# Optimization experiments

Hardware: AMD Instinct MI355X
Metric: run time of the kernel (lower is better)

## Reference

```python
import jax, jax.numpy as jnp
import numpy as np

NEG_INF = -jnp.inf


def setup_inputs() -> dict:
    key = jax.random.key(0)
    ks = jax.random.split(key, 8)
    B, C, H, W = 8, 512, 96, 96
    IC = max(1, C // 8)  # inter_channels = 64
    s = 1.0 / np.sqrt(C)
    x = jax.random.normal(ks[0], (B, C, H, W), dtype=jnp.float32)
    Wq = jax.random.normal(ks[1], (IC, C), dtype=jnp.float32) * s
    bq = jax.random.normal(ks[2], (IC,), dtype=jnp.float32) * s
    Wk = jax.random.normal(ks[3], (IC, C), dtype=jnp.float32) * s
    bk = jax.random.normal(ks[4], (IC,), dtype=jnp.float32) * s
    Wv = jax.random.normal(ks[5], (C, C), dtype=jnp.float32) * s
    bv = jax.random.normal(ks[6], (C,), dtype=jnp.float32) * s
    gamma = jnp.full((1,), 0.5, dtype=jnp.float32)  # nn.Parameter (zeros in torch; nonzero here for a non-trivial baseline)
    return {"x": x, "Wq": Wq, "bq": bq, "Wk": Wk, "bk": bk, "Wv": Wv, "bv": bv, "gamma": gamma}


def reference(x, Wq, bq, Wk, bk, Wv, bv, gamma):
    B, C, H, W = x.shape
    # 1x1 convs as channel contractions
    q = jnp.einsum('oc,bchw->bohw', Wq, x) + bq[None, :, None, None]
    k = jnp.einsum('oc,bchw->bohw', Wk, x) + bk[None, :, None, None]
    v = jnp.einsum('oc,bchw->bohw', Wv, x) + bv[None, :, None, None]
    # column (height-axis) attention logits: [B, H, W, H'] with -inf on h==h'
    e_h = jnp.einsum('bchw,bcgw->bhwg', q, k)
    eye = jnp.eye(H, dtype=bool)[:, None, :]  # [H,1,H'] broadcast over W
    e_h = jnp.where(eye[None], NEG_INF, e_h)
    # row (width-axis) attention logits: [B, H, W, W']
    e_w = jnp.einsum('bchw,bchv->bhwv', q, k)
    # joint softmax over concatenated H'+W' axis
    attn = jax.nn.softmax(jnp.concatenate([e_h, e_w], axis=-1), axis=-1)
    a_h = attn[..., :H]   # [B,H,W,H']
    a_w = attn[..., H:]   # [B,H,W,W']
    out_h = jnp.einsum('bcgw,bhwg->bchw', v, a_h)
    out_w = jnp.einsum('bchv,bhwv->bchw', v, a_w)
    return gamma[0] * (out_h + out_w) + x
```

## Files before the change

kernel.cpp:

```cpp
#include <hip/hip_runtime.h>
#include <hip/hip_bf16.h>

typedef __hip_bfloat16 bf16;
typedef unsigned short us8 __attribute__((ext_vector_type(8)));
typedef __attribute__((ext_vector_type(8))) short short8v;
typedef __attribute__((ext_vector_type(4))) float float4v;

__device__ __forceinline__ float us2f(unsigned short u){
  return __uint_as_float(((unsigned int)u) << 16);
}
__device__ __forceinline__ float b2f(bf16 v){ return __bfloat162float(v); }
__device__ __forceinline__ bf16 f2b(float v){ return __float2bfloat16(v); }
__device__ __forceinline__ unsigned short f2bu(float v){
  bf16 t = f2b(v); return *reinterpret_cast<unsigned short*>(&t);
}

#define HW 9216
#define CH 512
#define NQ 640

__global__ void k_detect(const unsigned int* __restrict__ xw, int* __restrict__ flag){
  int t = threadIdx.x;
  int cnt = 0;
  for(int i=t;i<4096;i+=256){
    unsigned e = (xw[i]>>8)&0x7F;
    if(e==0x3E||e==0x3F) cnt++;
  }
  #pragma unroll
  for(int o=32;o>0;o>>=1) cnt += __shfl_xor(cnt,o);
  __shared__ int s[4];
  if((t&63)==0) s[t>>6]=cnt;
  __syncthreads();
  if(t==0){ int tot=s[0]+s[1]+s[2]+s[3]; *flag = (tot > 1228) ? 1 : 0; }
}

__global__ void k_pack(const void* __restrict__ Wq, const void* __restrict__ Wk,
                       const void* __restrict__ Wv, const void* __restrict__ bq,
                       const void* __restrict__ bk, const void* __restrict__ bv,
                       const int* __restrict__ flag,
                       bf16* __restrict__ Wall, float* __restrict__ ball){
  bool isbf = (*flag)!=0;
  int j = blockIdx.x, t = threadIdx.x;
  const void* src = (j < 64) ? Wq : (j < 128) ? Wk : Wv;
  int row = (j < 64) ? j : (j < 128) ? (j-64) : (j-128);
  for(int c=t;c<512;c+=256){
    float v = isbf ? b2f(((const bf16*)src)[(size_t)row*512+c])
                   : ((const float*)src)[(size_t)row*512+c];
    Wall[(size_t)j*512+c] = f2b(v);
  }
  if(t==0){
    const void* bsrc = (j<64)? bq : (j<128)? bk : bv;
    ball[j] = isbf ? b2f(((const bf16*)bsrc)[row]) : ((const float*)bsrc)[row];
  }
}

__global__ __launch_bounds__(256) void k_xcvt(const void* __restrict__ x,
    const int* __restrict__ flag, bf16* __restrict__ xT){
  __shared__ float T[64][65];
  bool isbf = (*flag)!=0;
  int b = blockIdx.z, c0 = blockIdx.y*64, hw0 = blockIdx.x*64;
  int tid = threadIdx.x;
  if(isbf){
    const bf16* xb = (const bf16*)x + ((size_t)b*CH + c0)*HW + hw0;
    #pragma unroll
    for(int i=0;i<2;i++){
      int e = i*256 + tid;
      int cc = e>>3, h8 = (e&7)*8;
      us8 v = *(const us8*)(xb + (size_t)cc*HW + h8);
      #pragma unroll
      for(int j=0;j<8;j++) T[cc][h8+j] = us2f(v[j]);
    }
  } else {
    const float* xb = (const float*)x + ((size_t)b*CH + c0)*HW + hw0;
    #pragma unroll
    for(int i=0;i<4;i++){
      int e = i*256 + tid;
      int cc = e>>4, h4 = (e&15)*4;
      float4 v = *(const float4*)(xb + (size_t)cc*HW + h4);
      T[cc][h4]=v.x; T[cc][h4+1]=v.y; T[cc][h4+2]=v.z; T[cc][h4+3]=v.w;
    }
  }
  __syncthreads();
  bf16* tb = xT + ((size_t)b*HW + hw0)*512 + c0;
  #pragma unroll
  for(int i=0;i<2;i++){
    int e = i*256 + tid;
    int r = e>>3, c8 = (e&7)*8;
    us8 o;
    #pragma unroll
    for(int j=0;j<8;j++) o[j] = f2bu(T[c8+j][r]);
    *(us8*)(tb + (size_t)r*512 + c8) = o;
  }
}

__global__ __launch_bounds__(256) void k_qkv(const bf16* __restrict__ xT,
    const bf16* __restrict__ Wall, const float* __restrict__ ball,
    bf16* __restrict__ Ot){
  __shared__ ushort As[128][72];
  __shared__ ushort Bs[128][72];
  int b = blockIdx.y;
  int bx = blockIdx.x;
  int swz = (bx & 7)*45 + (bx >> 3);
  int m0 = (swz/5)*128;
  int n0 = (swz%5)*128;
  int tid = threadIdx.x, wid = tid>>6, lane = tid&63;
  int m0w = (wid>>1)*64, n0w = (wid&1)*64;
  const bf16* Ab = xT + ((size_t)b*HW + m0)*512;
  const bf16* Bb = Wall + (size_t)n0*512;
  float4v acc[4][4];
  #pragma unroll
  for(int mt=0;mt<4;mt++)
    #pragma unroll
    for(int nt=0;nt<4;nt++) acc[mt][nt] = (float4v){0.f,0.f,0.f,0.f};
  for(int k0=0;k0<512;k0+=64){
    #pragma unroll
    for(int i=0;i<4;i++){
      int s = tid + i*256;
      int row = s>>3, ko = (s&7)*8;
      us8 v = *(const us8*)(Ab + (size_t)row*512 + k0 + ko);
      *(us8*)&As[row][ko] = v;
      us8 w = *(const us8*)(Bb + (size_t)row*512 + k0 + ko);
      *(us8*)&Bs[row][ko] = w;
    }
    __syncthreads();
    #pragma unroll
    for(int kk=0;kk<64;kk+=32){
      short8v a[4], bb[4];
      #pragma unroll
      for(int mt=0;mt<4;mt++) a[mt] = *(short8v*)&As[m0w+mt*16+(lane&15)][kk+8*(lane>>4)];
      #pragma unroll
      for(int nt=0;nt<4;nt++) bb[nt] = *(short8v*)&Bs[n0w+nt*16+(lane&15)][kk+8*(lane>>4)];
      #pragma unroll
      for(int mt=0;mt<4;mt++)
        #pragma unroll
        for(int nt=0;nt<4;nt++)
          acc[mt][nt] = __builtin_amdgcn_mfma_f32_16x16x32_bf16(a[mt], bb[nt], acc[mt][nt], 0,0,0);
    }
    __syncthreads();
  }
  #pragma unroll
  for(int mt=0;mt<4;mt++){
    #pragma unroll
    for(int nt=0;nt<4;nt++){
      int nn = n0 + n0w + nt*16 + (lane&15);
      float bias = ball[nn];
      int mbase = m0 + m0w + mt*16 + (lane>>4)*4;
      #pragma unroll
      for(int r=0;r<4;r++)
        Ot[((size_t)b*HW + mbase + r)*640 + nn] = f2b(acc[mt][nt][r] + bias);
    }
  }
}

__global__ __launch_bounds__(384) void k_eh(const bf16* __restrict__ Ot,
                                            float* __restrict__ esc){
  __shared__ ushort Qs[96][72];
  __shared__ ushort Ks[96][72];
  int b = blockIdx.y, w = blockIdx.x;
  int tid = threadIdx.x, wid = tid>>6, lane = tid&63;
  const bf16* qb = Ot + ((size_t)b*HW + w)*640;
  #pragma unroll
  for(int i=0;i<2;i++){
    int e = tid + i*384;
    int row = e>>3, ko = (e&7)*8;
    us8 q = *(const us8*)(qb + (size_t)row*96*640 + ko);
    *(us8*)&Qs[row][ko] = q;
    us8 k = *(const us8*)(qb + (size_t)row*96*640 + 64 + ko);
    *(us8*)&Ks[row][ko] = k;
  }
  __syncthreads();
  float4v acc[6];
  #pragma unroll
  for(int nt=0;nt<6;nt++) acc[nt] = (float4v){0.f,0.f,0.f,0.f};
  #pragma unroll
  for(int kt=0;kt<2;kt++){
    int kb = kt*32 + 8*(lane>>4);
    short8v a = *(short8v*)&Qs[wid*16 + (lane&15)][kb];
    #pragma unroll
    for(int nt=0;nt<6;nt++){
      short8v bb = *(short8v*)&Ks[nt*16 + (lane&15)][kb];
      acc[nt] = __builtin_amdgcn_mfma_f32_16x16x32_bf16(a, bb, acc[nt], 0,0,0);
    }
  }
  int hbase = wid*16 + (lane>>4)*4;
  #pragma unroll
  for(int nt=0;nt<6;nt++){
    int g = nt*16 + (lane&15);
    #pragma unroll
    for(int r=0;r<4;r++){
      int h = hbase + r;
      esc[((size_t)b*HW + (size_t)h*96 + w)*192 + g] =
          (g==h) ? -INFINITY : acc[nt][r];
    }
  }
}

__global__ __launch_bounds__(384) void k_ew(const bf16* __restrict__ Ot,
                                            float* __restrict__ esc){
  __shared__ ushort Qs[96][72];
  __shared__ ushort Ks[96][72];
  int b = blockIdx.y, h = blockIdx.x;
  int tid = threadIdx.x, wid = tid>>6, lane = tid&63;
  const bf16* qb = Ot + ((size_t)b*HW + (size_t)h*96)*640;
  #pragma unroll
  for(int i=0;i<2;i++){
    int e = tid + i*384;
    int row = e>>3, ko = (e&7)*8;
    us8 q = *(const us8*)(qb + (size_t)row*640 + ko);
    *(us8*)&Qs[row][ko] = q;
    us8 k = *(const us8*)(qb + (size_t)row*640 + 64 + ko);
    *(us8*)&Ks[row][ko] = k;
  }
  __syncthreads();
  float4v acc[6];
  #pragma unroll
  for(int nt=0;nt<6;nt++) acc[nt] = (float4v){0.f,0.f,0.f,0.f};
  #pragma unroll
  for(int kt=0;kt<2;kt++){
    int kb = kt*32 + 8*(lane>>4);
    short8v a = *(short8v*)&Qs[wid*16 + (lane&15)][kb];
    #pragma unroll
    for(int nt=0;nt<6;nt++){
      short8v bb = *(short8v*)&Ks[nt*16 + (lane&15)][kb];
      acc[nt] = __builtin_amdgcn_mfma_f32_16x16x32_bf16(a, bb, acc[nt], 0,0,0);
    }
  }
  int wbase = wid*16 + (lane>>4)*4;
  float* eb = esc + ((size_t)b*HW + (size_t)h*96)*192;
  #pragma unroll
  for(int nt=0;nt<6;nt++){
    int v = nt*16 + (lane&15);
    #pragma unroll
    for(int r=0;r<4;r++)
      eb[(size_t)(wbase + r)*192 + 96 + v] = acc[nt][r];
  }
}

__global__ __launch_bounds__(256) void k_sm(const float* __restrict__ esc,
                                            bf16* __restrict__ att){
  int tid = threadIdx.x, wave = tid>>6, lane = tid&63;
  size_t row0 = (size_t)blockIdx.x*16 + (size_t)wave*4;
  for(int r=0;r<4;r++){
    size_t row = row0 + r;
    const float* e = esc + row*192;
    float v0=e[lane], v1=e[lane+64], v2=e[lane+128];
    float m = fmaxf(fmaxf(v0,v1),v2);
    #pragma unroll
    for(int o=32;o>0;o>>=1) m = fmaxf(m, __shfl_xor(m,o));
    v0=__expf(v0-m); v1=__expf(v1-m); v2=__expf(v2-m);
    float s = v0+v1+v2;
    #pragma unroll
    for(int o=32;o>0;o>>=1) s += __shfl_xor(s,o);
    float inv = 1.0f/s;
    bf16* a = att + row*192;
    a[lane]=f2b(v0*inv); a[lane+64]=f2b(v1*inv); a[lane+128]=f2b(v2*inv);
  }
}

__global__ __launch_bounds__(384) void k_outw(const bf16* __restrict__ Ot,
    const bf16* __restrict__ att, bf16* __restrict__ P){
  __shared__ ushort As[96][104];
  __shared__ ushort Bs[128][104];
  int b = blockIdx.y;
  int h = blockIdx.x >> 2, c0 = (blockIdx.x & 3)*128;
  int tid = threadIdx.x, wid = tid>>6, lane = tid&63;
  const bf16* ab = att + ((size_t)b*HW + (size_t)h*96)*192 + 96;
  #pragma unroll
  for(int i=0;i<3;i++){
    int s = tid + i*384;
    int row = s/12, ko = (s%12)*8;
    us8 v = *(const us8*)(ab + (size_t)row*192 + ko);
    *(us8*)&As[row][ko] = v;
  }
  const bf16* vb = Ot + ((size_t)b*HW + (size_t)h*96)*640 + 128 + c0;
  #pragma unroll
  for(int i=0;i<4;i++){
    int s = tid + i*384;
    int g = s % 96, cc = s / 96;
    us8 v = *(const us8*)(vb + (size_t)g*640 + cc*8);
    #pragma unroll
    for(int j=0;j<8;j++) Bs[cc*8+j][g] = v[j];
  }
  __syncthreads();
  float4v acc[8];
  #pragma unroll
  for(int nt=0;nt<8;nt++) acc[nt] = (float4v){0.f,0.f,0.f,0.f};
  #pragma unroll
  for(int kt=0;kt<3;kt++){
    int kb = kt*32 + 8*(lane>>4);
    short8v a = *(short8v*)&As[wid*16 + (lane&15)][kb];
    #pragma unroll
    for(int nt=0;nt<8;nt++){
      short8v bb = *(short8v*)&Bs[nt*16 + (lane&15)][kb];
      acc[nt] = __builtin_amdgcn_mfma_f32_16x16x32_bf16(a, bb, acc[nt], 0,0,0);
    }
  }
  bf16* Pb = P + ((size_t)b*HW + (size_t)h*96)*512 + c0;
  int mb = wid*16 + (lane>>4)*4;
  #pragma unroll
  for(int nt=0;nt<8;nt++){
    int n = nt*16 + (lane&15);
    #pragma unroll
    for(int r=0;r<4;r++)
      Pb[(size_t)(mb + r)*512 + n] = f2b(acc[nt][r]);
  }
}

__global__ __launch_bounds__(384) void k_outh(const bf16* __restrict__ Ot,
    const bf16* __restrict__ att, bf16* __restrict__ P){
  __shared__ ushort As[96][104];
  __shared__ ushort Bs[128][104];
  int b = blockIdx.y;
  int w = blockIdx.x >> 2, c0 = (blockIdx.x & 3)*128;
  int tid = threadIdx.x, wid = tid>>6, lane = tid&63;
  const bf16* ab = att + ((size_t)b*HW + w)*192;
  #pragma unroll
  for(int i=0;i<3;i++){
    int s = tid + i*384;
    int row = s/12, ko = (s%12)*8;
    us8 v = *(const us8*)(ab + (size_t)row*96*192 + ko);
    *(us8*)&As[row][ko] = v;
  }
  const bf16* vb = Ot + ((size_t)b*HW + w)*640 + 128 + c0;
  #pragma unroll
  for(int i=0;i<4;i++){
    int s = tid + i*384;
    int g = s % 96, cc = s / 96;
    us8 v = *(const us8*)(vb + (size_t)g*96*640 + cc*8);
    #pragma unroll
    for(int j=0;j<8;j++) Bs[cc*8+j][g] = v[j];
  }
  __syncthreads();
  float4v acc[8];
  #pragma unroll
  for(int nt=0;nt<8;nt++) acc[nt] = (float4v){0.f,0.f,0.f,0.f};
  #pragma unroll
  for(int kt=0;kt<3;kt++){
    int kb = kt*32 + 8*(lane>>4);
    short8v a = *(short8v*)&As[wid*16 + (lane&15)][kb];
    #pragma unroll
    for(int nt=0;nt<8;nt++){
      short8v bb = *(short8v*)&Bs[nt*16 + (lane&15)][kb];
      acc[nt] = __builtin_amdgcn_mfma_f32_16x16x32_bf16(a, bb, acc[nt], 0,0,0);
    }
  }
  bf16* Pb = P + ((size_t)b*HW + w)*512 + c0;
  int mb = wid*16 + (lane>>4)*4;
  #pragma unroll
  for(int nt=0;nt<8;nt++){
    int n = nt*16 + (lane&15);
    #pragma unroll
    for(int r=0;r<4;r++){
      size_t o = (size_t)(mb + r)*96*512 + n;
      Pb[o] = f2b(b2f(Pb[o]) + acc[nt][r]);
    }
  }
}

__global__ __launch_bounds__(256) void k_final(const bf16* __restrict__ P,
    const void* __restrict__ x, const void* __restrict__ gamma,
    const int* __restrict__ flag, void* __restrict__ out){
  __shared__ float T[64][65];
  bool isbf = (*flag)!=0;
  int b = blockIdx.z; int hw0 = blockIdx.x*64; int c0 = blockIdx.y*64;
  int tid = threadIdx.x;
  float g = isbf ? b2f(((const bf16*)gamma)[0]) : ((const float*)gamma)[0];
  const bf16* Pb = P + ((size_t)b*HW + hw0)*CH + c0;
  #pragma unroll
  for(int i=0;i<2;i++){
    int e = i*256 + tid;
    int r = e>>3, c8 = (e&7)*8;
    us8 v = *(const us8*)(Pb + (size_t)r*CH + c8);
    #pragma unroll
    for(int j=0;j<8;j++) T[c8+j][r] = us2f(v[j]);
  }
  __syncthreads();
  if(isbf){
    const bf16* xb = (const bf16*)x + ((size_t)b*CH + c0)*HW + hw0;
    bf16* ob = (bf16*)out + ((size_t)b*CH + c0)*HW + hw0;
    #pragma unroll
    for(int i=0;i<2;i++){
      int e = i*256 + tid;
      int cc = e>>3, h8 = (e&7)*8;
      us8 xv = *(const us8*)(xb + (size_t)cc*HW + h8);
      us8 o;
      #pragma unroll
      for(int j=0;j<8;j++) o[j] = f2bu(g*T[cc][h8+j] + us2f(xv[j]));
      *(us8*)(ob + (size_t)cc*HW + h8) = o;
    }
  } else {
    const float* xb = (const float*)x + ((size_t)b*CH + c0)*HW + hw0;
    float* ob = (float*)out + ((size_t)b*CH + c0)*HW + hw0;
    #pragma unroll
    for(int i=0;i<4;i++){
      int e = i*256 + tid;
      int cc = e>>4, h4 = (e&15)*4;
      float4 xv = *(const float4*)(xb + (size_t)cc*HW + h4);
      float4 o;
      o.x = g*T[cc][h4]   + xv.x;
      o.y = g*T[cc][h4+1] + xv.y;
      o.z = g*T[cc][h4+2] + xv.z;
      o.w = g*T[cc][h4+3] + xv.w;
      *(float4*)(ob + (size_t)cc*HW + h4) = o;
    }
  }
}

extern "C" void kernel_launch(void* const* d_in, const int* in_sizes, int n_in,
                              void* d_out, int out_size, void* d_ws, size_t ws_size,
                              hipStream_t stream){
  (void)in_sizes; (void)n_in; (void)out_size; (void)ws_size;
  const void* x     = d_in[0];
  const void* Wq    = d_in[1];
  const void* bq    = d_in[2];
  const void* Wk    = d_in[3];
  const void* bk    = d_in[4];
  const void* Wv    = d_in[5];
  const void* bv    = d_in[6];
  const void* gamma = d_in[7];
  char* ws = (char*)d_ws;

  bf16*  Wall = (bf16*)(ws + 0);
  float* ball = (float*)(ws + 655360);
  int*   flag = (int*)(ws + 657920);
  bf16*  Ot   = (bf16*)(ws + (1u<<20));
  bf16*  att  = (bf16*)(ws + 95420416ull);
  bf16*  xT   = (bf16*)(ws + 123731968ull);
  float* esc  = (float*)(ws + 123731968ull);
  bf16*  P    = (bf16*)(ws + 123731968ull);

  hipLaunchKernelGGL(k_detect, dim3(1),       dim3(256), 0, stream,
                     (const unsigned int*)x, flag);
  hipLaunchKernelGGL(k_pack,   dim3(640),     dim3(256), 0, stream,
                     Wq, Wk, Wv, bq, bk, bv, flag, Wall, ball);
  hipLaunchKernelGGL(k_xcvt,   dim3(144,8,8), dim3(256), 0, stream, x, flag, xT);
  hipLaunchKernelGGL(k_qkv,    dim3(360,8),   dim3(256), 0, stream, xT, Wall, ball, Ot);
  hipLaunchKernelGGL(k_eh,     dim3(96,8),    dim3(384), 0, stream, Ot, esc);
  hipLaunchKernelGGL(k_ew,     dim3(96,8),    dim3(384), 0, stream, Ot, esc);
  hipLaunchKernelGGL(k_sm,     dim3(4608),    dim3(256), 0, stream, esc, att);
  hipLaunchKernelGGL(k_outw,   dim3(384,8),   dim3(384), 0, stream, Ot, att, P);
  hipLaunchKernelGGL(k_outh,   dim3(384,8),   dim3(384), 0, stream, Ot, att, P);
  hipLaunchKernelGGL(k_final,  dim3(144,8,8), dim3(256), 0, stream, P, x, gamma, flag, d_out);
}
```

Baseline: 314.3 us.

## Fuse row-logit and softmax kernels; use direct-to-LDS swizzled loads in QKV GEMM

The width-axis logit kernel now keeps its logits in shared memory and performs the joint softmax directly. It reads the height-axis logits from a smaller 96-wide buffer, which removes the separate softmax kernel and the round trip of the 192-wide fp32 logit array. The QKV GEMM also switches to global_load_lds 16-byte loads into an XOR-swizzled, unpadded LDS layout to avoid the register staging and bank conflicts. The softmax now runs on only 768 blocks with serial rows per wave, so it may lose parallelism, and the swizzle has to match between writers and readers.

```diff
diff --git a/kernel.cpp b/kernel.cpp
--- a/kernel.cpp
+++ b/kernel.cpp
@@ -13,6 +13,10 @@
 __device__ __forceinline__ bf16 f2b(float v){ return __float2bfloat16(v); }
 __device__ __forceinline__ unsigned short f2bu(float v){
   bf16 t = f2b(v); return *reinterpret_cast<unsigned short*>(&t);
+}
+__device__ __forceinline__ void gload16(const void* g, void* l){
+  __builtin_amdgcn_global_load_lds((const __attribute__((address_space(1))) void*)g,
+                                   (__attribute__((address_space(3))) void*)l, 16, 0, 0);
 }
 
 #define HW 9216
@@ -96,8 +100,8 @@
 __global__ __launch_bounds__(256) void k_qkv(const bf16* __restrict__ xT,
     const bf16* __restrict__ Wall, const float* __restrict__ ball,
     bf16* __restrict__ Ot){
-  __shared__ ushort As[128][72];
-  __shared__ ushort Bs[128][72];
+  __shared__ ushort AsL[128*64];
+  __shared__ ushort BsL[128*64];
   int b = blockIdx.y;
   int bx = blockIdx.x;
   int swz = (bx & 7)*45 + (bx >> 3);
@@ -107,6 +111,8 @@
   int m0w = (wid>>1)*64, n0w = (wid&1)*64;
   const bf16* Ab = xT + ((size_t)b*HW + m0)*512;
   const bf16* Bb = Wall + (size_t)n0*512;
+  int r8 = lane>>3, c8 = lane&7;
+  int csw = ((c8 ^ r8)*8);
   float4v acc[4][4];
   #pragma unroll
   for(int mt=0;mt<4;mt++)
@@ -114,22 +120,27 @@
     for(int nt=0;nt<4;nt++) acc[mt][nt] = (float4v){0.f,0.f,0.f,0.f};
   for(int k0=0;k0<512;k0+=64){
     #pragma unroll
-    for(int i=0;i<4;i++){
-      int s = tid + i*256;
-      int row = s>>3, ko = (s&7)*8;
-      us8 v = *(const us8*)(Ab + (size_t)row*512 + k0 + ko);
-      *(us8*)&As[row][ko] = v;
-      us8 w = *(const us8*)(Bb + (size_t)row*512 + k0 + ko);
-      *(us8*)&Bs[row][ko] = w;
+    for(int j=0;j<4;j++){
+      int row0 = (j*4 + wid)*8;
+      gload16(Ab + (size_t)(row0 + r8)*512 + k0 + csw, &AsL[row0*64]);
+      gload16(Bb + (size_t)(row0 + r8)*512 + k0 + csw, &BsL[row0*64]);
     }
     __syncthreads();
     #pragma unroll
     for(int kk=0;kk<64;kk+=32){
       short8v a[4], bb[4];
       #pragma unroll
-      for(int mt=0;mt<4;mt++) a[mt] = *(short8v*)&As[m0w+mt*16+(lane&15)][kk+8*(lane>>4)];
-      #pragma unroll
-      for(int nt=0;nt<4;nt++) bb[nt] = *(short8v*)&Bs[n0w+nt*16+(lane&15)][kk+8*(lane>>4)];
+      for(int mt=0;mt<4;mt++){
+        int row = m0w + mt*16 + (lane&15);
+        int kb = (kk*2 + 16*(lane>>4)) ^ ((row&7)<<4);
+        a[mt] = *(const short8v*)((const char*)AsL + row*128 + kb);
+      }
+      #pragma unroll
+      for(int nt=0;nt<4;nt++){
+        int row = n0w + nt*16 + (lane&15);
+        int kb = (kk*2 + 16*(lane>>4)) ^ ((row&7)<<4);
+        bb[nt] = *(const short8v*)((const char*)BsL + row*128 + kb);
+      }
       #pragma unroll
       for(int mt=0;mt<4;mt++)
         #pragma unroll
@@ -153,7 +164,7 @@
 }
 
 __global__ __launch_bounds__(384) void k_eh(const bf16* __restrict__ Ot,
-                                            float* __restrict__ esc){
+                                            float* __restrict__ eh2){
   __shared__ ushort Qs[96][72];
   __shared__ ushort Ks[96][72];
   int b = blockIdx.y, w = blockIdx.x;
@@ -189,16 +200,17 @@
     #pragma unroll
     for(int r=0;r<4;r++){
       int h = hbase + r;
-      esc[((size_t)b*HW + (size_t)h*96 + w)*192 + g] =
+      eh2[((size_t)b*HW + (size_t)h*96 + w)*96 + g] =
           (g==h) ? -INFINITY : acc[nt][r];
     }
   }
 }
 
-__global__ __launch_bounds__(384) void k_ew(const bf16* __restrict__ Ot,
-                                            float* __restrict__ esc){
+__global__ __launch_bounds__(384) void k_ewsm(const bf16* __restrict__ Ot,
+    const float* __restrict__ eh2, bf16* __restrict__ att){
   __shared__ ushort Qs[96][72];
   __shared__ ushort Ks[96][72];
+  __shared__ float Ew[96][100];
   int b = blockIdx.y, h = blockIdx.x;
   int tid = threadIdx.x, wid = tid>>6, lane = tid&63;
   const bf16* qb = Ot + ((size_t)b*HW + (size_t)h*96)*640;
@@ -226,24 +238,21 @@
     }
   }
   int wbase = wid*16 + (lane>>4)*4;
-  float* eb = esc + ((size_t)b*HW + (size_t)h*96)*192;
   #pragma unroll
   for(int nt=0;nt<6;nt++){
     int v = nt*16 + (lane&15);
     #pragma unroll
-    for(int r=0;r<4;r++)
-      eb[(size_t)(wbase + r)*192 + 96 + v] = acc[nt][r];
-  }
-}
-
-__global__ __launch_bounds__(256) void k_sm(const float* __restrict__ esc,
-                                            bf16* __restrict__ att){
-  int tid = threadIdx.x, wave = tid>>6, lane = tid&63;
-  size_t row0 = (size_t)blockIdx.x*16 + (size_t)wave*4;
-  for(int r=0;r<4;r++){
-    size_t row = row0 + r;
-    const float* e = esc + row*192;
-    float v0=e[lane], v1=e[lane+64], v2=e[lane+128];
+    for(int r=0;r<4;r++) Ew[wbase+r][v] = acc[nt][r];
+  }
+  __syncthreads();
+  const float* ehb = eh2 + ((size_t)b*HW + (size_t)h*96)*96;
+  bf16* ab = att + ((size_t)b*HW + (size_t)h*96)*192;
+  for(int r=0;r<16;r++){
+    int w = wid*16 + r;
+    const float* er = ehb + (size_t)w*96;
+    float v0 = er[lane];
+    float v1 = (lane<32) ? er[64+lane] : Ew[w][lane-32];
+    float v2 = Ew[w][lane+32];
     float m = fmaxf(fmaxf(v0,v1),v2);
     #pragma unroll
     for(int o=32;o>0;o>>=1) m = fmaxf(m, __shfl_xor(m,o));
@@ -252,7 +261,7 @@
     #pragma unroll
     for(int o=32;o>0;o>>=1) s += __shfl_xor(s,o);
     float inv = 1.0f/s;
-    bf16* a = att + row*192;
+    bf16* a = ab + (size_t)w*192;
     a[lane]=f2b(v0*inv); a[lane+64]=f2b(v1*inv); a[lane+128]=f2b(v2*inv);
   }
 }
@@ -426,7 +435,7 @@
   bf16*  Ot   = (bf16*)(ws + (1u<<20));
   bf16*  att  = (bf16*)(ws + 95420416ull);
   bf16*  xT   = (bf16*)(ws + 123731968ull);
-  float* esc  = (float*)(ws + 123731968ull);
+  float* eh2  = (float*)(ws + 123731968ull);
   bf16*  P    = (bf16*)(ws + 123731968ull);
 
   hipLaunchKernelGGL(k_detect, dim3(1),       dim3(256), 0, stream,
@@ -435,9 +444,8 @@
                      Wq, Wk, Wv, bq, bk, bv, flag, Wall, ball);
   hipLaunchKernelGGL(k_xcvt,   dim3(144,8,8), dim3(256), 0, stream, x, flag, xT);
   hipLaunchKernelGGL(k_qkv,    dim3(360,8),   dim3(256), 0, stream, xT, Wall, ball, Ot);
-  hipLaunchKernelGGL(k_eh,     dim3(96,8),    dim3(384), 0, stream, Ot, esc);
-  hipLaunchKernelGGL(k_ew,     dim3(96,8),    dim3(384), 0, stream, Ot, esc);
-  hipLaunchKernelGGL(k_sm,     dim3(4608),    dim3(256), 0, stream, esc, att);
+  hipLaunchKernelGGL(k_eh,     dim3(96,8),    dim3(384), 0, stream, Ot, eh2);
+  hipLaunchKernelGGL(k_ewsm,   dim3(96,8),    dim3(384), 0, stream, Ot, eh2, att);
   hipLaunchKernelGGL(k_outw,   dim3(384,8),   dim3(384), 0, stream, Ot, att, P);
   hipLaunchKernelGGL(k_outh,   dim3(384,8),   dim3(384), 0, stream, Ot, att, P);
   hipLaunchKernelGGL(k_final,  dim3(144,8,8), dim3(256), 0, stream, P, x, gamma, flag, d_out);
```

New measurement: 332.2 us. 5.7% more time.
